# Kernel tuning notes

Hardware: AMD Instinct MI355X
Metric: run time of the kernel (lower is better)

Reference implementation:

```python
import jax, jax.numpy as jnp
import numpy as np

HQ, HKV = 16, 4          # query heads, kv heads
ROPE_BASE = 10000.0


def _rope(t, positions):
    # t: [B, H, S, hd]; standard rotate-half RoPE over head_dim
    hd = t.shape[-1]
    inv_freq = 1.0 / (ROPE_BASE ** (jnp.arange(0, hd, 2, dtype=jnp.float32) / hd))
    freqs = positions.astype(jnp.float32)[:, None] * inv_freq[None, :]      # [S, hd/2]
    emb = jnp.concatenate([freqs, freqs], axis=-1)                           # [S, hd]
    cos = jnp.cos(emb)[None, None, :, :].astype(t.dtype)
    sin = jnp.sin(emb)[None, None, :, :].astype(t.dtype)
    t1, t2 = t[..., : hd // 2], t[..., hd // 2 :]
    rot = jnp.concatenate([-t2, t1], axis=-1)
    return t * cos + rot * sin


def setup_inputs() -> dict:
    key = jax.random.key(0)
    k0, k1, k2, k3, k4 = jax.random.split(key, 5)
    B, S, D = 2, 2048, 2048
    hd = D // HQ
    x = jax.random.normal(k0, (B, S, D), dtype=jnp.float32)
    s = 0.02
    wq = jax.random.normal(k1, (HQ * hd, D), dtype=jnp.float32) * s
    wk = jax.random.normal(k2, (HKV * hd, D), dtype=jnp.float32) * s
    wv = jax.random.normal(k3, (HKV * hd, D), dtype=jnp.float32) * s
    wo = jax.random.normal(k4, (D, HQ * hd), dtype=jnp.float32) * s
    return {"x": x, "wq": wq, "wk": wk, "wv": wv, "wo": wo}


def reference(x, wq, wk, wv, wo):
    B, S, D = x.shape
    hd = D // HQ
    G = HQ // HKV
    positions = jnp.arange(S)

    q = (x @ wq.T).reshape(B, S, HQ, hd).transpose(0, 2, 1, 3)   # [B,Hq,S,hd]
    k = (x @ wk.T).reshape(B, S, HKV, hd).transpose(0, 2, 1, 3)  # [B,Hkv,S,hd]
    v = (x @ wv.T).reshape(B, S, HKV, hd).transpose(0, 2, 1, 3)

    q = _rope(q, positions)
    k = _rope(k, positions)

    # GQA: expand KV heads to match query heads (repeat_interleave on head dim)
    k = jnp.repeat(k, G, axis=1)
    v = jnp.repeat(v, G, axis=1)

    scores = jnp.einsum("bhqd,bhkd->bhqk", q, k) / jnp.sqrt(jnp.float32(hd))
    causal = jnp.tril(jnp.ones((S, S), dtype=bool))
    scores = jnp.where(causal[None, None], scores, -jnp.inf)
    attn = jax.nn.softmax(scores, axis=-1)

    out = jnp.einsum("bhqk,bhkd->bhqd", attn, v)                 # [B,Hq,S,hd]
    out = out.transpose(0, 2, 1, 3).reshape(B, S, HQ * hd)
    return out @ wo.T
```

## Files before the change

kernel.cpp:

```cpp
#include <hip/hip_runtime.h>

#define B_   2
#define S_   2048
#define D_   2048
#define HQ_  16
#define HKV_ 4
#define HD_  128

typedef __attribute__((ext_vector_type(4))) float f32x4;
typedef __attribute__((ext_vector_type(4))) short s16x4;
typedef __attribute__((ext_vector_type(8))) short s16x8;

static __device__ __forceinline__ ushort f2bf(float f) {
  uint32_t u = __float_as_uint(f);
  u += 0x7fffu + ((u >> 16) & 1u);
  return (ushort)(u >> 16);
}

static __device__ __forceinline__ s16x8 mk8(s16x4 lo, s16x4 hi) {
  s16x8 r;
  r[0] = lo[0]; r[1] = lo[1]; r[2] = lo[2]; r[3] = lo[3];
  r[4] = hi[0]; r[5] = hi[1]; r[6] = hi[2]; r[7] = hi[3];
  return r;
}

static __device__ __forceinline__ void gload16(const ushort* g, ushort* l) {
  __builtin_amdgcn_global_load_lds((const __attribute__((address_space(1))) uint32_t*)(g),
                                   (__attribute__((address_space(3))) uint32_t*)(l), 16, 0, 0);
}

__global__ void cast_kernel(const float* __restrict__ in, ushort* __restrict__ out, int n) {
  int i = (blockIdx.x * blockDim.x + threadIdx.x) * 4;
  if (i + 3 < n) {
    float4 v = *(const float4*)(in + i);
    *(ushort4*)(out + i) = make_ushort4(f2bf(v.x), f2bf(v.y), f2bf(v.z), f2bf(v.w));
  }
}

__global__ __launch_bounds__(256) void gemm_nt_bf16(const ushort* __restrict__ A,
                                                    const ushort* __restrict__ Bm,
                                                    float* __restrict__ C,
                                                    int M, int N, int K) {
  __shared__ ushort As[128 * 64];
  __shared__ ushort Bs[128 * 64];
  const int tid  = threadIdx.x;
  const int lane = tid & 63;
  const int wave = tid >> 6;
  const int lrow = lane & 15, lgrp = lane >> 4;
  const int wm = (wave >> 1) * 64, wn = (wave & 1) * 64;
  const int brow = blockIdx.y * 128, bcol = blockIdx.x * 128;

  f32x4 acc[4][4];
#pragma unroll
  for (int i = 0; i < 4; ++i)
#pragma unroll
    for (int j = 0; j < 4; ++j) acc[i][j] = (f32x4){0.f, 0.f, 0.f, 0.f};

  const int r_ = tid >> 3, c16 = tid & 7;
  const ushort* Abase = A + (size_t)brow * K;
  const ushort* Bbase = Bm + (size_t)bcol * K;

  for (int k0 = 0; k0 < K; k0 += 64) {
#pragma unroll
    for (int q = 0; q < 4; ++q) {
      const int row = q * 32 + r_;
      const int sc = c16 ^ (row & 7);
      gload16(Abase + (size_t)row * K + k0 + sc * 8, &As[q * 2048 + wave * 512]);
      gload16(Bbase + (size_t)row * K + k0 + sc * 8, &Bs[q * 2048 + wave * 512]);
    }
    __syncthreads();
#pragma unroll
    for (int kc = 0; kc < 2; ++kc) {
      s16x8 aF[4], bF[4];
#pragma unroll
      for (int mt = 0; mt < 4; ++mt) {
        const int row = wm + mt * 16 + lrow;
        aF[mt] = *(const s16x8*)&As[row * 64 + ((kc * 32 + lgrp * 8) ^ ((row & 7) << 3))];
      }
#pragma unroll
      for (int nt = 0; nt < 4; ++nt) {
        const int row = wn + nt * 16 + lrow;
        bF[nt] = *(const s16x8*)&Bs[row * 64 + ((kc * 32 + lgrp * 8) ^ ((row & 7) << 3))];
      }
#pragma unroll
      for (int mt = 0; mt < 4; ++mt)
#pragma unroll
        for (int nt = 0; nt < 4; ++nt)
          acc[mt][nt] = __builtin_amdgcn_mfma_f32_16x16x32_bf16(aF[mt], bF[nt], acc[mt][nt], 0, 0, 0);
    }
    __syncthreads();
  }
#pragma unroll
  for (int mt = 0; mt < 4; ++mt) {
#pragma unroll
    for (int nt = 0; nt < 4; ++nt) {
      const int row = brow + wm + mt * 16 + lgrp * 4;
      const int col = bcol + wn + nt * 16 + lrow;
#pragma unroll
      for (int rr = 0; rr < 4; ++rr)
        C[(size_t)(row + rr) * N + col] = acc[mt][nt][rr];
    }
  }
}

__global__ void rope_qk(const float* __restrict__ qkv, ushort* __restrict__ Qb, ushort* __restrict__ Kb) {
  int idx = blockIdx.x * 256 + threadIdx.x;
  int i  = idx & 63;
  int t  = idx >> 6;
  int h2 = t % 20;
  int t2 = t / 20;
  int s  = t2 & (S_ - 1);
  int b  = t2 >> 11;
  float inv = exp2f(-(float)i * 0.20762050594046832f);
  float f = (float)s * inv;
  float sn, cs;
  sincosf(f, &sn, &cs);
  size_t row = (size_t)(b * S_ + s) * 3072;
  if (h2 < HQ_) {
    int h = h2;
    float a = qkv[row + h * 128 + i];
    float c2 = qkv[row + h * 128 + i + 64];
    size_t ob = ((size_t)((b * HQ_ + h) * S_ + s)) * 128;
    Qb[ob + i]      = f2bf(a * cs - c2 * sn);
    Qb[ob + i + 64] = f2bf(c2 * cs + a * sn);
  } else {
    int kh = h2 - HQ_;
    float a = qkv[row + 2048 + kh * 128 + i];
    float c2 = qkv[row + 2048 + kh * 128 + i + 64];
    size_t ob = ((size_t)((b * HKV_ + kh) * S_ + s)) * 128;
    Kb[ob + i]      = f2bf(a * cs - c2 * sn);
    Kb[ob + i + 64] = f2bf(c2 * cs + a * sn);
  }
}

__global__ __launch_bounds__(256) void v_transpose(const float* __restrict__ qkv, ushort* __restrict__ Vt) {
  __shared__ ushort tile[128][72];
  const int s0 = blockIdx.x * 64;
  const int kh = blockIdx.y;
  const int b  = blockIdx.z;
  for (int idx = threadIdx.x; idx < 64 * 128; idx += 256) {
    int sl = idx >> 7;
    int d  = idx & 127;
    float v = qkv[(size_t)(b * S_ + s0 + sl) * 3072 + 2560 + kh * 128 + d];
    tile[d][sl] = f2bf(v);
  }
  __syncthreads();
  for (int idx = threadIdx.x; idx < 64 * 128; idx += 256) {
    int d  = idx >> 6;
    int sl = idx & 63;
    Vt[((size_t)(b * HKV_ + kh) * 128 + d) * S_ + s0 + sl] = tile[d][sl];
  }
}

__global__ __launch_bounds__(256) void attn_kernel(const ushort* __restrict__ Qb,
                                                   const ushort* __restrict__ Kb,
                                                   const ushort* __restrict__ Vt,
                                                   ushort* __restrict__ Ao) {
  __shared__ ushort Qs[64 * 128];
  __shared__ ushort Ks[64 * 128];
  __shared__ ushort Vts[128 * 64];
  const int h  = blockIdx.y;
  const int b  = blockIdx.z;
  const int kh = h >> 2;
  const int tid = threadIdx.x, lane = tid & 63, wave = tid >> 6;
  const int lrow = lane & 15, lgrp = lane >> 4;
  const int sw = (lrow & 7) << 3;
  const float NEGINF = -3.0e38f;
  const float SCL2 = 0.12751744717f;

#pragma unroll 1
  for (int hf = 0; hf < 2; ++hf) {
    const int qt = hf ? (31 - (int)blockIdx.x) : (int)blockIdx.x;
    const int q0 = qt * 64;

    {
      const int r = tid >> 2;
      const int swr = (r & 7) << 3;
      const ushort* src = Qb + (((size_t)(b * HQ_ + h)) * S_ + q0 + r) * HD_ + (tid & 3) * 32;
#pragma unroll
      for (int q = 0; q < 4; ++q) {
        const int u = (tid & 3) * 32 + q * 8;
        *(s16x8*)&Qs[r * 128 + (u ^ swr)] = *(const s16x8*)(src + q * 8);
      }
    }
    __syncthreads();
    s16x8 qF[4];
#pragma unroll
    for (int c = 0; c < 4; ++c)
      qF[c] = *(const s16x8*)&Qs[(wave * 16 + lrow) * 128 + ((c * 32 + lgrp * 8) ^ sw)];

    float m_run = NEGINF, l_run = 0.f;
    f32x4 o[8];
#pragma unroll
    for (int dt = 0; dt < 8; ++dt) o[dt] = (f32x4){0.f, 0.f, 0.f, 0.f};
    const int qg = q0 + wave * 16 + lrow;

    for (int kt = 0; kt <= qt; ++kt) {
      {
        const int r = tid >> 2;
        const int swr = (r & 7) << 3;
        const ushort* src = Kb + (((size_t)(b * HKV_ + kh)) * S_ + kt * 64 + r) * HD_ + (tid & 3) * 32;
#pragma unroll
        for (int q = 0; q < 4; ++q) {
          const int u = (tid & 3) * 32 + q * 8;
          *(s16x8*)&Ks[r * 128 + (u ^ swr)] = *(const s16x8*)(src + q * 8);
        }
      }
      {
        const int r = tid >> 1;
        const int swr = (r & 7) << 3;
        const ushort* src = Vt + ((size_t)(b * HKV_ + kh) * 128 + r) * S_ + kt * 64 + (tid & 1) * 32;
#pragma unroll
        for (int q = 0; q < 4; ++q) {
          const int u = (tid & 1) * 32 + q * 8;
          *(s16x8*)&Vts[r * 64 + (u ^ swr)] = *(const s16x8*)(src + q * 8);
        }
      }
      __syncthreads();

      f32x4 sF[4];
#pragma unroll
      for (int hh = 0; hh < 4; ++hh) {
        f32x4 a = (f32x4){0.f, 0.f, 0.f, 0.f};
#pragma unroll
        for (int c = 0; c < 4; ++c) {
          const s16x8 kA = *(const s16x8*)&Ks[(hh * 16 + lrow) * 128 + ((c * 32 + lgrp * 8) ^ sw)];
          a = __builtin_amdgcn_mfma_f32_16x16x32_bf16(kA, qF[c], a, 0, 0, 0);
        }
        sF[hh] = a;
      }

      float p[16];
      float tmax = NEGINF;
      if (kt == qt) {
#pragma unroll
        for (int hh = 0; hh < 4; ++hh)
#pragma unroll
          for (int rr = 0; rr < 4; ++rr) {
            const int kg = kt * 64 + hh * 16 + lgrp * 4 + rr;
            const float s = (kg <= qg) ? sF[hh][rr] * SCL2 : NEGINF;
            p[hh * 4 + rr] = s;
            tmax = fmaxf(tmax, s);
          }
      } else {
#pragma unroll
        for (int hh = 0; hh < 4; ++hh)
#pragma unroll
          for (int rr = 0; rr < 4; ++rr) {
            const float s = sF[hh][rr] * SCL2;
            p[hh * 4 + rr] = s;
            tmax = fmaxf(tmax, s);
          }
      }
      tmax = fmaxf(tmax, __shfl_xor(tmax, 16, 64));
      tmax = fmaxf(tmax, __shfl_xor(tmax, 32, 64));
      const float m_new = fmaxf(m_run, tmax);
      const float alpha = exp2f(m_run - m_new);
      float psum = 0.f;
#pragma unroll
      for (int i = 0; i < 16; ++i) {
        p[i] = exp2f(p[i] - m_new);
        psum += p[i];
      }
      psum += __shfl_xor(psum, 16, 64);
      psum += __shfl_xor(psum, 32, 64);
      l_run = l_run * alpha + psum;
      m_run = m_new;

      float alphaR[4];
#pragma unroll
      for (int rr = 0; rr < 4; ++rr) alphaR[rr] = __shfl(alpha, lgrp * 4 + rr, 64);
#pragma unroll
      for (int dt = 0; dt < 8; ++dt)
#pragma unroll
        for (int rr = 0; rr < 4; ++rr) o[dt][rr] *= alphaR[rr];

      s16x8 pa0, pa1;
#pragma unroll
      for (int j = 0; j < 8; ++j) { pa0[j] = (short)f2bf(p[j]); pa1[j] = (short)f2bf(p[8 + j]); }

#pragma unroll
      for (int dt = 0; dt < 8; ++dt) {
        const int vr = dt * 16 + lrow;
        s16x8 v0 = mk8(*(const s16x4*)&Vts[vr * 64 + ((lgrp * 4) ^ sw)],
                       *(const s16x4*)&Vts[vr * 64 + ((lgrp * 4 + 16) ^ sw)]);
        s16x8 v1 = mk8(*(const s16x4*)&Vts[vr * 64 + ((32 + lgrp * 4) ^ sw)],
                       *(const s16x4*)&Vts[vr * 64 + ((32 + lgrp * 4 + 16) ^ sw)]);
        o[dt] = __builtin_amdgcn_mfma_f32_16x16x32_bf16(pa0, v0, o[dt], 0, 0, 0);
        o[dt] = __builtin_amdgcn_mfma_f32_16x16x32_bf16(pa1, v1, o[dt], 0, 0, 0);
      }
      __syncthreads();
    }

    float lR[4];
#pragma unroll
    for (int rr = 0; rr < 4; ++rr) lR[rr] = 1.f / __shfl(l_run, lgrp * 4 + rr, 64);
#pragma unroll
    for (int dt = 0; dt < 8; ++dt)
#pragma unroll
      for (int rr = 0; rr < 4; ++rr) {
        const int s = q0 + wave * 16 + lgrp * 4 + rr;
        Ao[(size_t)(b * S_ + s) * D_ + h * HD_ + dt * 16 + lrow] = f2bf(o[dt][rr] * lR[rr]);
      }
  }
}

extern "C" void kernel_launch(void* const* d_in, const int* in_sizes, int n_in,
                              void* d_out, int out_size, void* d_ws, size_t ws_size,
                              hipStream_t stream) {
  const float* x  = (const float*)d_in[0];
  const float* wq = (const float*)d_in[1];
  const float* wk = (const float*)d_in[2];
  const float* wv = (const float*)d_in[3];
  const float* wo = (const float*)d_in[4];
  float* out = (float*)d_out;
  char* ws = (char*)d_ws;

  ushort* xb    = (ushort*)(ws);
  ushort* wqkvb = (ushort*)(ws + 16777216);
  ushort* wob   = (ushort*)(ws + 29360128);
  float*  qkvf  = (float*) (ws + 37748736);
  ushort* Qb    = (ushort*)(ws + 88080384);
  ushort* Kb    = (ushort*)(ws + 104857600);
  ushort* Vt    = (ushort*)(ws + 109051904);
  ushort* Ao    = (ushort*)(ws + 113246208);

  cast_kernel<<<8192, 256, 0, stream>>>(x,  xb, 8388608);
  cast_kernel<<<4096, 256, 0, stream>>>(wq, wqkvb, 4194304);
  cast_kernel<<<1024, 256, 0, stream>>>(wk, wqkvb + 4194304, 1048576);
  cast_kernel<<<1024, 256, 0, stream>>>(wv, wqkvb + 5242880, 1048576);
  cast_kernel<<<4096, 256, 0, stream>>>(wo, wob, 4194304);

  gemm_nt_bf16<<<dim3(24, 32), 256, 0, stream>>>(xb, wqkvb, qkvf, 4096, 3072, 2048);
  rope_qk<<<20480, 256, 0, stream>>>(qkvf, Qb, Kb);
  v_transpose<<<dim3(32, 4, 2), 256, 0, stream>>>(qkvf, Vt);
  attn_kernel<<<dim3(16, 16, 2), 256, 0, stream>>>(Qb, Kb, Vt, Ao);
  gemm_nt_bf16<<<dim3(16, 32), 256, 0, stream>>>(Ao, wob, out, 4096, 2048, 2048);
}
```

Before: 357.6 us.

## Rewrite attention with 32x32 MFMA, double-buffered async KV loads, lazy rescale; remap GEMM grid

The attention kernel now uses 128-row query tiles with 32x32x16 bf16 MFMAs. Q stays in registers and K/V tiles are double-buffered through direct global-to-LDS loads, so the next tile loads while the current one computes. The softmax scale is folded into Q during RoPE, and V columns are permuted during the transpose so packed P can feed the MFMA directly. The max rescale is skipped when the running max grows by less than a threshold. The GEMMs get a 1D grid with an XCD-aware block remap to improve L2 locality. These changes aim to raise MFMA efficiency and hide load latency, at the cost of higher register pressure and occupancy limited to one block per CU.

After: 347.8 us. 1.03x faster.

```diff
diff --git a/kernel.cpp b/kernel.cpp
--- a/kernel.cpp
+++ b/kernel.cpp
@@ -8,6 +8,7 @@
 #define HD_  128
 
 typedef __attribute__((ext_vector_type(4))) float f32x4;
+typedef __attribute__((ext_vector_type(16))) float f32x16;
 typedef __attribute__((ext_vector_type(4))) short s16x4;
 typedef __attribute__((ext_vector_type(8))) short s16x8;
 
@@ -15,13 +16,6 @@
   uint32_t u = __float_as_uint(f);
   u += 0x7fffu + ((u >> 16) & 1u);
   return (ushort)(u >> 16);
-}
-
-static __device__ __forceinline__ s16x8 mk8(s16x4 lo, s16x4 hi) {
-  s16x8 r;
-  r[0] = lo[0]; r[1] = lo[1]; r[2] = lo[2]; r[3] = lo[3];
-  r[4] = hi[0]; r[5] = hi[1]; r[6] = hi[2]; r[7] = hi[3];
-  return r;
 }
 
 static __device__ __forceinline__ void gload16(const ushort* g, ushort* l) {
@@ -40,15 +34,20 @@
 __global__ __launch_bounds__(256) void gemm_nt_bf16(const ushort* __restrict__ A,
                                                     const ushort* __restrict__ Bm,
                                                     float* __restrict__ C,
-                                                    int M, int N, int K) {
+                                                    int M, int N, int K, int nbx) {
   __shared__ ushort As[128 * 64];
   __shared__ ushort Bs[128 * 64];
+  const int nwg = gridDim.x;
+  const int per = nwg >> 3;
+  const int id = blockIdx.x;
+  const int wg = (id & 7) * per + (id >> 3);
+  const int bx = wg % nbx, by = wg / nbx;
   const int tid  = threadIdx.x;
   const int lane = tid & 63;
   const int wave = tid >> 6;
   const int lrow = lane & 15, lgrp = lane >> 4;
   const int wm = (wave >> 1) * 64, wn = (wave & 1) * 64;
-  const int brow = blockIdx.y * 128, bcol = blockIdx.x * 128;
+  const int brow = by * 128, bcol = bx * 128;
 
   f32x4 acc[4][4];
 #pragma unroll
@@ -117,12 +116,13 @@
   sincosf(f, &sn, &cs);
   size_t row = (size_t)(b * S_ + s) * 3072;
   if (h2 < HQ_) {
+    const float SCL2 = 0.12751744716705736f;
     int h = h2;
     float a = qkv[row + h * 128 + i];
     float c2 = qkv[row + h * 128 + i + 64];
     size_t ob = ((size_t)((b * HQ_ + h) * S_ + s)) * 128;
-    Qb[ob + i]      = f2bf(a * cs - c2 * sn);
-    Qb[ob + i + 64] = f2bf(c2 * cs + a * sn);
+    Qb[ob + i]      = f2bf((a * cs - c2 * sn) * SCL2);
+    Qb[ob + i + 64] = f2bf((c2 * cs + a * sn) * SCL2);
   } else {
     int kh = h2 - HQ_;
     float a = qkv[row + 2048 + kh * 128 + i];
@@ -148,160 +148,160 @@
   for (int idx = threadIdx.x; idx < 64 * 128; idx += 256) {
     int d  = idx >> 6;
     int sl = idx & 63;
-    Vt[((size_t)(b * HKV_ + kh) * 128 + d) * S_ + s0 + sl] = tile[d][sl];
-  }
-}
-
-__global__ __launch_bounds__(256) void attn_kernel(const ushort* __restrict__ Qb,
-                                                   const ushort* __restrict__ Kb,
-                                                   const ushort* __restrict__ Vt,
-                                                   ushort* __restrict__ Ao) {
-  __shared__ ushort Qs[64 * 128];
-  __shared__ ushort Ks[64 * 128];
-  __shared__ ushort Vts[128 * 64];
-  const int h  = blockIdx.y;
-  const int b  = blockIdx.z;
-  const int kh = h >> 2;
+    int sp = (sl & 48) | (sl & 3) | ((sl & 8) >> 1) | ((sl & 4) << 1);
+    Vt[((size_t)(b * HKV_ + kh) * 128 + d) * S_ + s0 + sp] = tile[d][sl];
+  }
+}
+
+__global__ __launch_bounds__(256, 1) void attn_kernel(const ushort* __restrict__ Qb,
+                                                      const ushort* __restrict__ Kb,
+                                                      const ushort* __restrict__ Vt,
+                                                      ushort* __restrict__ Ao) {
+  __shared__ ushort Ks[2][64 * 128];
+  __shared__ ushort Vs[2][128 * 64];
+  const int h = blockIdx.y, b = blockIdx.z, kh = h >> 2;
   const int tid = threadIdx.x, lane = tid & 63, wave = tid >> 6;
-  const int lrow = lane & 15, lgrp = lane >> 4;
-  const int sw = (lrow & 7) << 3;
-  const float NEGINF = -3.0e38f;
-  const float SCL2 = 0.12751744717f;
+  const int lq = lane & 31, g = lane >> 5;
+  const ushort* Kg = Kb + ((size_t)(b * HKV_ + kh)) * S_ * HD_;
+  const ushort* Vg = Vt + ((size_t)(b * HKV_ + kh)) * HD_ * S_;
 
 #pragma unroll 1
-  for (int hf = 0; hf < 2; ++hf) {
-    const int qt = hf ? (31 - (int)blockIdx.x) : (int)blockIdx.x;
-    const int q0 = qt * 64;
-
+  for (int half = 0; half < 2; ++half) {
+    const int qt = half ? (15 - (int)blockIdx.x) : (int)blockIdx.x;
+    const int q0 = qt * 128;
+    const int qg = q0 + wave * 32 + lq;
+    const int nk = 2 * qt + 2;
+
+    s16x8 qF[8];
     {
-      const int r = tid >> 2;
-      const int swr = (r & 7) << 3;
-      const ushort* src = Qb + (((size_t)(b * HQ_ + h)) * S_ + q0 + r) * HD_ + (tid & 3) * 32;
-#pragma unroll
-      for (int q = 0; q < 4; ++q) {
-        const int u = (tid & 3) * 32 + q * 8;
-        *(s16x8*)&Qs[r * 128 + (u ^ swr)] = *(const s16x8*)(src + q * 8);
-      }
-    }
+      const ushort* qrow = Qb + (((size_t)(b * HQ_ + h)) * S_ + q0 + wave * 32 + lq) * HD_ + g * 8;
+#pragma unroll
+      for (int s = 0; s < 8; ++s) qF[s] = *(const s16x8*)(qrow + s * 16);
+    }
+
+#define STAGE(buf, kt64)                                                          \
+    {                                                                             \
+      _Pragma("unroll")                                                           \
+      for (int i_ = 0; i_ < 4; ++i_) {                                            \
+        const int slot = i_ * 256 + tid;                                          \
+        const int r = slot >> 4, c = slot & 15;                                   \
+        const int cc = c ^ (r & 15);                                              \
+        gload16(Kg + ((size_t)((kt64) * 64 + r)) * HD_ + cc * 8,                  \
+                &Ks[buf][i_ * 2048 + wave * 512]);                                \
+      }                                                                           \
+      _Pragma("unroll")                                                           \
+      for (int i_ = 0; i_ < 4; ++i_) {                                            \
+        const int slot = i_ * 256 + tid;                                          \
+        const int r = slot >> 3, c = slot & 7;                                    \
+        const int cc = c ^ (r & 7);                                               \
+        gload16(Vg + (size_t)r * S_ + (kt64) * 64 + cc * 8,                       \
+                &Vs[buf][i_ * 2048 + wave * 512]);                                \
+      }                                                                           \
+    }
+
+    STAGE(0, 0);
+
+    f32x16 acc[4] = {};
+    float m_run = -3.0e38f, l_run = 0.f;
+
+    asm volatile("s_waitcnt vmcnt(0)" ::: "memory");
     __syncthreads();
-    s16x8 qF[4];
-#pragma unroll
-    for (int c = 0; c < 4; ++c)
-      qF[c] = *(const s16x8*)&Qs[(wave * 16 + lrow) * 128 + ((c * 32 + lgrp * 8) ^ sw)];
-
-    float m_run = NEGINF, l_run = 0.f;
-    f32x4 o[8];
-#pragma unroll
-    for (int dt = 0; dt < 8; ++dt) o[dt] = (f32x4){0.f, 0.f, 0.f, 0.f};
-    const int qg = q0 + wave * 16 + lrow;
-
-    for (int kt = 0; kt <= qt; ++kt) {
-      {
-        const int r = tid >> 2;
-        const int swr = (r & 7) << 3;
-        const ushort* src = Kb + (((size_t)(b * HKV_ + kh)) * S_ + kt * 64 + r) * HD_ + (tid & 3) * 32;
-#pragma unroll
-        for (int q = 0; q < 4; ++q) {
-          const int u = (tid & 3) * 32 + q * 8;
-          *(s16x8*)&Ks[r * 128 + (u ^ swr)] = *(const s16x8*)(src + q * 8);
+
+    for (int kt = 0; kt < nk; ++kt) {
+      const int cur = kt & 1;
+      if (kt + 1 < nk) STAGE(cur ^ 1, kt + 1);
+      const ushort* Kc = &Ks[cur][0];
+      const ushort* Vc = &Vs[cur][0];
+
+      f32x16 sacc[2];
+#pragma unroll
+      for (int t = 0; t < 2; ++t) {
+        f32x16 a = {};
+        const int row = t * 32 + lq;
+#pragma unroll
+        for (int s = 0; s < 8; ++s) {
+          const int cc = (s * 2 + g) ^ (row & 15);
+          const s16x8 kA = *(const s16x8*)(Kc + row * 128 + cc * 8);
+          a = __builtin_amdgcn_mfma_f32_32x32x16_bf16(kA, qF[s], a, 0, 0, 0);
         }
-      }
-      {
-        const int r = tid >> 1;
-        const int swr = (r & 7) << 3;
-        const ushort* src = Vt + ((size_t)(b * HKV_ + kh) * 128 + r) * S_ + kt * 64 + (tid & 1) * 32;
-#pragma unroll
-        for (int q = 0; q < 4; ++q) {
-          const int u = (tid & 1) * 32 + q * 8;
-          *(s16x8*)&Vts[r * 64 + (u ^ swr)] = *(const s16x8*)(src + q * 8);
-        }
-      }
-      __syncthreads();
-
-      f32x4 sF[4];
-#pragma unroll
-      for (int hh = 0; hh < 4; ++hh) {
-        f32x4 a = (f32x4){0.f, 0.f, 0.f, 0.f};
-#pragma unroll
-        for (int c = 0; c < 4; ++c) {
-          const s16x8 kA = *(const s16x8*)&Ks[(hh * 16 + lrow) * 128 + ((c * 32 + lgrp * 8) ^ sw)];
-          a = __builtin_amdgcn_mfma_f32_16x16x32_bf16(kA, qF[c], a, 0, 0, 0);
-        }
-        sF[hh] = a;
-      }
-
-      float p[16];
-      float tmax = NEGINF;
-      if (kt == qt) {
-#pragma unroll
-        for (int hh = 0; hh < 4; ++hh)
-#pragma unroll
-          for (int rr = 0; rr < 4; ++rr) {
-            const int kg = kt * 64 + hh * 16 + lgrp * 4 + rr;
-            const float s = (kg <= qg) ? sF[hh][rr] * SCL2 : NEGINF;
-            p[hh * 4 + rr] = s;
-            tmax = fmaxf(tmax, s);
+        sacc[t] = a;
+      }
+
+      float tmax = -3.0e38f;
+      if (kt >= 2 * qt) {
+#pragma unroll
+        for (int t = 0; t < 2; ++t)
+#pragma unroll
+          for (int r = 0; r < 16; ++r) {
+            const int kg = kt * 64 + t * 32 + (r & 3) + 8 * (r >> 2) + 4 * g;
+            if (kg > qg) sacc[t][r] = -3.0e38f;
+            tmax = fmaxf(tmax, sacc[t][r]);
           }
       } else {
 #pragma unroll
-        for (int hh = 0; hh < 4; ++hh)
-#pragma unroll
-          for (int rr = 0; rr < 4; ++rr) {
-            const float s = sF[hh][rr] * SCL2;
-            p[hh * 4 + rr] = s;
-            tmax = fmaxf(tmax, s);
-          }
-      }
-      tmax = fmaxf(tmax, __shfl_xor(tmax, 16, 64));
+        for (int t = 0; t < 2; ++t)
+#pragma unroll
+          for (int r = 0; r < 16; ++r) tmax = fmaxf(tmax, sacc[t][r]);
+      }
       tmax = fmaxf(tmax, __shfl_xor(tmax, 32, 64));
-      const float m_new = fmaxf(m_run, tmax);
-      const float alpha = exp2f(m_run - m_new);
+
+      if (!__all(tmax <= m_run + 8.f)) {
+        const float m_new = fmaxf(m_run, tmax);
+        const float alpha = exp2f(m_run - m_new);
+        m_run = m_new;
+        l_run *= alpha;
+#pragma unroll
+        for (int dt = 0; dt < 4; ++dt)
+#pragma unroll
+          for (int r = 0; r < 16; ++r) acc[dt][r] *= alpha;
+      }
+
       float psum = 0.f;
-#pragma unroll
-      for (int i = 0; i < 16; ++i) {
-        p[i] = exp2f(p[i] - m_new);
-        psum += p[i];
-      }
-      psum += __shfl_xor(psum, 16, 64);
+      uint32_t pk[16];
+#pragma unroll
+      for (int t = 0; t < 2; ++t)
+#pragma unroll
+        for (int i = 0; i < 8; ++i) {
+          const float e0 = exp2f(sacc[t][2 * i]     - m_run);
+          const float e1 = exp2f(sacc[t][2 * i + 1] - m_run);
+          psum += e0 + e1;
+          asm("v_cvt_pk_bf16_f32 %0, %1, %2" : "=v"(pk[t * 8 + i]) : "v"(e0), "v"(e1));
+        }
       psum += __shfl_xor(psum, 32, 64);
-      l_run = l_run * alpha + psum;
-      m_run = m_new;
-
-      float alphaR[4];
-#pragma unroll
-      for (int rr = 0; rr < 4; ++rr) alphaR[rr] = __shfl(alpha, lgrp * 4 + rr, 64);
-#pragma unroll
-      for (int dt = 0; dt < 8; ++dt)
-#pragma unroll
-        for (int rr = 0; rr < 4; ++rr) o[dt][rr] *= alphaR[rr];
-
-      s16x8 pa0, pa1;
-#pragma unroll
-      for (int j = 0; j < 8; ++j) { pa0[j] = (short)f2bf(p[j]); pa1[j] = (short)f2bf(p[8 + j]); }
-
-#pragma unroll
-      for (int dt = 0; dt < 8; ++dt) {
-        const int vr = dt * 16 + lrow;
-        s16x8 v0 = mk8(*(const s16x4*)&Vts[vr * 64 + ((lgrp * 4) ^ sw)],
-                       *(const s16x4*)&Vts[vr * 64 + ((lgrp * 4 + 16) ^ sw)]);
-        s16x8 v1 = mk8(*(const s16x4*)&Vts[vr * 64 + ((32 + lgrp * 4) ^ sw)],
-                       *(const s16x4*)&Vts[vr * 64 + ((32 + lgrp * 4 + 16) ^ sw)]);
-        o[dt] = __builtin_amdgcn_mfma_f32_16x16x32_bf16(pa0, v0, o[dt], 0, 0, 0);
-        o[dt] = __builtin_amdgcn_mfma_f32_16x16x32_bf16(pa1, v1, o[dt], 0, 0, 0);
-      }
+      l_run += psum;
+
+#pragma unroll
+      for (int ks = 0; ks < 4; ++ks) {
+        union { s16x8 v; uint32_t u[4]; } pb;
+#pragma unroll
+        for (int j = 0; j < 4; ++j) pb.u[j] = pk[ks * 4 + j];
+#pragma unroll
+        for (int dt = 0; dt < 4; ++dt) {
+          const int row = dt * 32 + lq;
+          const int cc = (ks * 2 + g) ^ (row & 7);
+          const s16x8 vA = *(const s16x8*)(Vc + row * 64 + cc * 8);
+          acc[dt] = __builtin_amdgcn_mfma_f32_32x32x16_bf16(vA, pb.v, acc[dt], 0, 0, 0);
+        }
+      }
+
+      asm volatile("s_waitcnt vmcnt(0)" ::: "memory");
       __syncthreads();
     }
 
-    float lR[4];
-#pragma unroll
-    for (int rr = 0; rr < 4; ++rr) lR[rr] = 1.f / __shfl(l_run, lgrp * 4 + rr, 64);
-#pragma unroll
-    for (int dt = 0; dt < 8; ++dt)
-#pragma unroll
-      for (int rr = 0; rr < 4; ++rr) {
-        const int s = q0 + wave * 16 + lgrp * 4 + rr;
-        Ao[(size_t)(b * S_ + s) * D_ + h * HD_ + dt * 16 + lrow] = f2bf(o[dt][rr] * lR[rr]);
-      }
+    const float inv_l = 1.f / l_run;
+    ushort* orow = Ao + ((size_t)(b * S_ + qg)) * D_ + h * HD_;
+#pragma unroll
+    for (int dt = 0; dt < 4; ++dt)
+#pragma unroll
+      for (int u = 0; u < 4; ++u) {
+        ushort4 w;
+        w.x = f2bf(acc[dt][4 * u + 0] * inv_l);
+        w.y = f2bf(acc[dt][4 * u + 1] * inv_l);
+        w.z = f2bf(acc[dt][4 * u + 2] * inv_l);
+        w.w = f2bf(acc[dt][4 * u + 3] * inv_l);
+        *(ushort4*)(orow + dt * 32 + 8 * u + 4 * g) = w;
+      }
+#undef STAGE
   }
 }
 
@@ -331,9 +331,9 @@
   cast_kernel<<<1024, 256, 0, stream>>>(wv, wqkvb + 5242880, 1048576);
   cast_kernel<<<4096, 256, 0, stream>>>(wo, wob, 4194304);
 
-  gemm_nt_bf16<<<dim3(24, 32), 256, 0, stream>>>(xb, wqkvb, qkvf, 4096, 3072, 2048);
+  gemm_nt_bf16<<<768, 256, 0, stream>>>(xb, wqkvb, qkvf, 4096, 3072, 2048, 24);
   rope_qk<<<20480, 256, 0, stream>>>(qkvf, Qb, Kb);
   v_transpose<<<dim3(32, 4, 2), 256, 0, stream>>>(qkvf, Vt);
-  attn_kernel<<<dim3(16, 16, 2), 256, 0, stream>>>(Qb, Kb, Vt, Ao);
-  gemm_nt_bf16<<<dim3(16, 32), 256, 0, stream>>>(Ao, wob, out, 4096, 2048, 2048);
-}
+  attn_kernel<<<dim3(8, 16, 2), 256, 0, stream>>>(Qb, Kb, Vt, Ao);
+  gemm_nt_bf16<<<512, 256, 0, stream>>>(Ao, wob, out, 4096, 2048, 2048, 16);
+}
```
